# Optimization experiments

Hardware: AMD Instinct MI355X
Metric: run time of the kernel (lower is better)

The kernel has to match this reference:

```python
import jax, jax.numpy as jnp
import numpy as np

N_NODES = 50000
N_EDGES = 640000
D = 128
OUT = 1


def setup_inputs() -> dict:
    key = jax.random.key(0)
    k1, k2, k3, k4 = jax.random.split(key, 4)
    X = jax.random.normal(k1, (N_NODES, D), dtype=jnp.float32)
    edge_index = jax.random.randint(k2, (2, N_EDGES), 0, N_NODES, dtype=jnp.int64)
    W1 = jax.random.normal(k3, (OUT, D), dtype=jnp.float32) / np.sqrt(D)
    W2 = jax.random.normal(k4, (OUT, D), dtype=jnp.float32) / np.sqrt(D)
    return {"X": X, "edge_index": edge_index, "W1": W1, "W2": W2}


def reference(X, edge_index, W1, W2):
    # E[e] = W1 @ X[src[e]] + W2 @ X[dst[e]]
    # Gather endpoint features then apply the two bias-free linears and add.
    src, dst = edge_index[0], edge_index[1]
    Xs = X[src]                      # [E, D]
    Xd = X[dst]                      # [E, D]
    return jnp.einsum('ed,od->eo', Xs, W1) + jnp.einsum('ed,od->eo', Xd, W2)  # [E, OUT]
```

## Files before the change

kernel.cpp:

```cpp
#include <hip/hip_runtime.h>

#define N_NODES 50000
#define N_EDGES 640000
#define D 128

typedef float  f4 __attribute__((ext_vector_type(4)));
typedef int    i4 __attribute__((ext_vector_type(4)));

__global__ __launch_bounds__(256) void node_scores_kernel(
    const float* __restrict__ X,
    const float* __restrict__ W1,
    const float* __restrict__ W2,
    float* __restrict__ s1,
    float* __restrict__ s2)
{
    const int lane = threadIdx.x & 63;
    const int sl   = lane & 15;
    const int sub  = lane >> 4;
    const int wave = blockIdx.x * (blockDim.x >> 6) + (threadIdx.x >> 6);
    const int n    = wave * 4 + sub;
    if (n >= N_NODES) return;

    const f4* W1v = (const f4*)W1;
    const f4* W2v = (const f4*)W2;
    const f4 w1a = W1v[sl * 2],     w1b = W1v[sl * 2 + 1];
    const f4 w2a = W2v[sl * 2],     w2b = W2v[sl * 2 + 1];

    const f4* Xv = (const f4*)(X + (size_t)n * D);
    const f4 x0 = __builtin_nontemporal_load(&Xv[sl * 2]);
    const f4 x1 = __builtin_nontemporal_load(&Xv[sl * 2 + 1]);

    float p1 = x0.x * w1a.x + x0.y * w1a.y + x0.z * w1a.z + x0.w * w1a.w
             + x1.x * w1b.x + x1.y * w1b.y + x1.z * w1b.z + x1.w * w1b.w;
    float p2 = x0.x * w2a.x + x0.y * w2a.y + x0.z * w2a.z + x0.w * w2a.w
             + x1.x * w2b.x + x1.y * w2b.y + x1.z * w2b.z + x1.w * w2b.w;

    #pragma unroll
    for (int off = 8; off > 0; off >>= 1) {
        p1 += __shfl_xor(p1, off, 64);
        p2 += __shfl_xor(p2, off, 64);
    }
    if (sl == 0) {
        s1[n] = p1;
        s2[n] = p2;
    }
}

__global__ __launch_bounds__(256) void edge_combine_kernel(
    const int* __restrict__ src,
    const int* __restrict__ dst,
    const float* __restrict__ s1,
    const float* __restrict__ s2,
    float* __restrict__ out)
{
    const int i = blockIdx.x * blockDim.x + threadIdx.x;
    if (i < N_EDGES / 4) {
        const i4 s = __builtin_nontemporal_load(&((const i4*)src)[i]);
        const i4 d = __builtin_nontemporal_load(&((const i4*)dst)[i]);
        f4 o;
        o.x = s1[s.x] + s2[d.x];
        o.y = s1[s.y] + s2[d.y];
        o.z = s1[s.z] + s2[d.z];
        o.w = s1[s.w] + s2[d.w];
        __builtin_nontemporal_store(o, &((f4*)out)[i]);
    }
}

extern "C" void kernel_launch(void* const* d_in, const int* in_sizes, int n_in,
                              void* d_out, int out_size, void* d_ws, size_t ws_size,
                              hipStream_t stream) {
    const float* X  = (const float*)d_in[0];
    const int*   ei = (const int*)d_in[1];
    const float* W1 = (const float*)d_in[2];
    const float* W2 = (const float*)d_in[3];
    float* out = (float*)d_out;

    float* s1 = (float*)d_ws;
    float* s2 = s1 + N_NODES;

    const int blocks1 = (N_NODES + 15) / 16;
    node_scores_kernel<<<blocks1, 256, 0, stream>>>(X, W1, W2, s1, s2);

    const int n4 = N_EDGES / 4;
    edge_combine_kernel<<<(n4 + 255) / 256, 256, 0, stream>>>(
        ei, ei + N_EDGES, s1, s2, out);
}
```

Before: 86.74 us.

## Fuse node-score and edge-combine kernels via cooperative grid sync

Merges the two kernels into one persistent cooperative kernel with 1024 blocks. Each block computes per-node scores in a grid-stride loop, then waits at a grid-wide barrier before gathering the edge scores. This removes the second launch and the gap between kernels, at the cost of a grid barrier and a cooperative launch that may carry its own overhead. Using fewer blocks may also lower the memory parallelism available to the streaming phases.

```diff
diff --git a/kernel.cpp b/kernel.cpp
--- a/kernel.cpp
+++ b/kernel.cpp
@@ -1,4 +1,7 @@
 #include <hip/hip_runtime.h>
+#include <hip/hip_cooperative_groups.h>
+
+namespace cg = cooperative_groups;
 
 #define N_NODES 50000
 #define N_EDGES 640000
@@ -7,54 +10,53 @@
 typedef float  f4 __attribute__((ext_vector_type(4)));
 typedef int    i4 __attribute__((ext_vector_type(4)));
 
-__global__ __launch_bounds__(256) void node_scores_kernel(
+__global__ __launch_bounds__(256) void fused_edge_decoder(
     const float* __restrict__ X,
+    const int*   __restrict__ src,
+    const int*   __restrict__ dst,
     const float* __restrict__ W1,
     const float* __restrict__ W2,
     float* __restrict__ s1,
-    float* __restrict__ s2)
+    float* __restrict__ s2,
+    float* __restrict__ out,
+    int total_groups)
 {
     const int lane = threadIdx.x & 63;
     const int sl   = lane & 15;
     const int sub  = lane >> 4;
     const int wave = blockIdx.x * (blockDim.x >> 6) + (threadIdx.x >> 6);
-    const int n    = wave * 4 + sub;
-    if (n >= N_NODES) return;
+    const int g    = wave * 4 + sub;
 
     const f4* W1v = (const f4*)W1;
     const f4* W2v = (const f4*)W2;
-    const f4 w1a = W1v[sl * 2],     w1b = W1v[sl * 2 + 1];
-    const f4 w2a = W2v[sl * 2],     w2b = W2v[sl * 2 + 1];
+    const f4 w1a = W1v[sl * 2], w1b = W1v[sl * 2 + 1];
+    const f4 w2a = W2v[sl * 2], w2b = W2v[sl * 2 + 1];
 
-    const f4* Xv = (const f4*)(X + (size_t)n * D);
-    const f4 x0 = __builtin_nontemporal_load(&Xv[sl * 2]);
-    const f4 x1 = __builtin_nontemporal_load(&Xv[sl * 2 + 1]);
+    for (int n = g; n < N_NODES; n += total_groups) {
+        const f4* Xv = (const f4*)(X + (size_t)n * D);
+        const f4 x0 = __builtin_nontemporal_load(&Xv[sl * 2]);
+        const f4 x1 = __builtin_nontemporal_load(&Xv[sl * 2 + 1]);
+        float p1 = x0.x * w1a.x + x0.y * w1a.y + x0.z * w1a.z + x0.w * w1a.w
+                 + x1.x * w1b.x + x1.y * w1b.y + x1.z * w1b.z + x1.w * w1b.w;
+        float p2 = x0.x * w2a.x + x0.y * w2a.y + x0.z * w2a.z + x0.w * w2a.w
+                 + x1.x * w2b.x + x1.y * w2b.y + x1.z * w2b.z + x1.w * w2b.w;
+        #pragma unroll
+        for (int off = 8; off > 0; off >>= 1) {
+            p1 += __shfl_xor(p1, off, 64);
+            p2 += __shfl_xor(p2, off, 64);
+        }
+        if (sl == 0) {
+            s1[n] = p1;
+            s2[n] = p2;
+        }
+    }
 
-    float p1 = x0.x * w1a.x + x0.y * w1a.y + x0.z * w1a.z + x0.w * w1a.w
-             + x1.x * w1b.x + x1.y * w1b.y + x1.z * w1b.z + x1.w * w1b.w;
-    float p2 = x0.x * w2a.x + x0.y * w2a.y + x0.z * w2a.z + x0.w * w2a.w
-             + x1.x * w2b.x + x1.y * w2b.y + x1.z * w2b.z + x1.w * w2b.w;
+    __threadfence();
+    cg::this_grid().sync();
 
-    #pragma unroll
-    for (int off = 8; off > 0; off >>= 1) {
-        p1 += __shfl_xor(p1, off, 64);
-        p2 += __shfl_xor(p2, off, 64);
-    }
-    if (sl == 0) {
-        s1[n] = p1;
-        s2[n] = p2;
-    }
-}
-
-__global__ __launch_bounds__(256) void edge_combine_kernel(
-    const int* __restrict__ src,
-    const int* __restrict__ dst,
-    const float* __restrict__ s1,
-    const float* __restrict__ s2,
-    float* __restrict__ out)
-{
-    const int i = blockIdx.x * blockDim.x + threadIdx.x;
-    if (i < N_EDGES / 4) {
+    const int nthreads = gridDim.x * blockDim.x;
+    const int tid = blockIdx.x * blockDim.x + threadIdx.x;
+    for (int i = tid; i < N_EDGES / 4; i += nthreads) {
         const i4 s = __builtin_nontemporal_load(&((const i4*)src)[i]);
         const i4 d = __builtin_nontemporal_load(&((const i4*)dst)[i]);
         f4 o;
@@ -78,10 +80,14 @@
     float* s1 = (float*)d_ws;
     float* s2 = s1 + N_NODES;
 
-    const int blocks1 = (N_NODES + 15) / 16;
-    node_scores_kernel<<<blocks1, 256, 0, stream>>>(X, W1, W2, s1, s2);
+    const int blocks = 1024;
+    const int total_groups = blocks * 16;
+    const int* src = ei;
+    const int* dst = ei + N_EDGES;
 
-    const int n4 = N_EDGES / 4;
-    edge_combine_kernel<<<(n4 + 255) / 256, 256, 0, stream>>>(
-        ei, ei + N_EDGES, s1, s2, out);
+    void* args[] = {(void*)&X, (void*)&src, (void*)&dst, (void*)&W1,
+                    (void*)&W2, (void*)&s1, (void*)&s2, (void*)&out,
+                    (void*)&total_groups};
+    hipLaunchCooperativeKernel((const void*)fused_edge_decoder,
+                               dim3(blocks), dim3(256), args, 0, stream);
 }
```

Result: slower. 228.1 us (+162.9%).
